# Kernel optimization log

Hardware: AMD Instinct MI355X
Metric: run time of the kernel (lower is better)

The kernel has to match this reference:

```python
import jax, jax.numpy as jnp
import numpy as np

D = 256; NH = 8; NL = 4; NP = 8; DFF = 1024; NQ = 300; BS = 8
DH = D // NH
_SHAPES = np.array([[100, 100], [50, 50], [25, 25], [13, 13]], dtype=np.int64)
S = int(_SHAPES.prod(1).sum())


def setup_inputs():
    key = jax.random.key(0)
    ks = jax.random.split(key, 24)
    rn = lambda k, sh, s=0.02: jax.random.normal(k, sh, jnp.float32) * s
    lsi = np.concatenate([[0], np.cumsum(_SHAPES.prod(1))[:-1]])
    return {
        'tgt': rn(ks[0], (NQ, BS, D), 1.0),
        'tgt_query_mask': rn(ks[1], (NQ, BS, D), 1.0),
        'tgt_reference_bboxs': jax.random.uniform(ks[2], (NQ, BS, 4), jnp.float32, 0.1, 0.5),
        'tgt_reference_masks': jax.random.uniform(ks[3], (NQ, BS, 32, 32), jnp.float32),
        'memory': rn(ks[4], (S, BS, D), 1.0),
        'in_proj_w': rn(ks[5], (3 * D, D)), 'in_proj_b': jnp.zeros((3 * D,), jnp.float32),
        'out_sa_w': rn(ks[6], (D, D)), 'out_sa_b': jnp.zeros((D,), jnp.float32),
        'norm2_g': jnp.ones((D,), jnp.float32), 'norm2_b': jnp.zeros((D,), jnp.float32),
        'value_w': rn(ks[7], (D, D)), 'value_b': jnp.zeros((D,), jnp.float32),
        'off_w': rn(ks[8], (NH * NL * NP * 2, D)), 'off_b': rn(ks[9], (NH * NL * NP * 2,), 0.5),
        'aw_w': rn(ks[10], (NH * NL * NP, D)), 'aw_b': jnp.zeros((NH * NL * NP,), jnp.float32),
        'out_ca_w': rn(ks[11], (D, D)), 'out_ca_b': jnp.zeros((D,), jnp.float32),
        'norm1_g': jnp.ones((D,), jnp.float32), 'norm1_b': jnp.zeros((D,), jnp.float32),
        'lin1_w': rn(ks[12], (DFF, D)), 'lin1_b': jnp.zeros((DFF,), jnp.float32),
        'lin2_w': rn(ks[13], (D, DFF)), 'lin2_b': jnp.zeros((D,), jnp.float32),
        'norm3_g': jnp.ones((D,), jnp.float32), 'norm3_b': jnp.zeros((D,), jnp.float32),
        'memory_key_padding_mask': jnp.zeros((BS, S), bool),
        'memory_spatial_shapes': jnp.asarray(_SHAPES, jnp.int32),
        'memory_level_start_index': jnp.asarray(lsi, jnp.int32),
    }


def _lin(x, w, b):
    return x @ w.T + b


def _ln(x, g, b):
    mu = x.mean(-1, keepdims=True)
    v = ((x - mu) ** 2).mean(-1, keepdims=True)
    return (x - mu) / jnp.sqrt(v + 1e-5) * g + b


def _ms_deform(query, ref, mem, pad_mask, spatial, lstart, vw, vb, ow, ob, aww, awb, outw, outb):
    # query/ref/mem: (bs, nq, D), (bs, nq, 4 cxcywh in [0,1]), (bs, S, D)
    bs, nq, _ = query.shape
    value = _lin(mem, vw, vb)
    value = jnp.where(pad_mask[:, :, None], 0.0, value).reshape(bs, -1, NH, DH)
    off = _lin(query, ow, ob).reshape(bs, nq, NH, NL, NP, 2)
    aw = jax.nn.softmax(_lin(query, aww, awb).reshape(bs, nq, NH, NL * NP), -1)
    aw = aw.reshape(bs, nq, NH, NL, NP)
    ref6 = ref[:, :, None, None, None, :]
    loc = ref6[..., :2] + off / NP * ref6[..., 2:4] * 0.5  # (bs,nq,NH,NL,NP,2)
    Hs = spatial[:, 0].reshape(1, 1, 1, NL, 1)
    Ws = spatial[:, 1].reshape(1, 1, 1, NL, 1)
    ls = lstart.reshape(1, 1, 1, NL, 1)
    Hf = Hs.astype(jnp.float32); Wf = Ws.astype(jnp.float32)
    # grid_sample align_corners=False pixel coords
    x = loc[..., 0] * Wf - 0.5
    y = loc[..., 1] * Hf - 0.5
    x0 = jnp.floor(x); y0 = jnp.floor(y)
    vT = value.transpose(2, 0, 1, 3)  # (NH,bs,S,DH)
    acc = jnp.zeros((bs, nq, NH, NL, NP, DH), jnp.float32)
    for dx in (0.0, 1.0):
        for dy in (0.0, 1.0):
            xi = x0 + dx; yi = y0 + dy
            w = (1.0 - jnp.abs(x - xi)) * (1.0 - jnp.abs(y - yi))
            valid = ((xi >= 0) & (xi < Wf) & (yi >= 0) & (yi < Hf)).astype(jnp.float32)
            xc = jnp.clip(xi, 0.0, Wf - 1.0).astype(jnp.int32)
            yc = jnp.clip(yi, 0.0, Hf - 1.0).astype(jnp.int32)
            idx = ls + yc * Ws + xc  # flat index into S, (bs,nq,NH,NL,NP)
            iT = idx.transpose(2, 0, 1, 3, 4).reshape(NH, bs, -1)
            g = jax.vmap(lambda v, i: jnp.take_along_axis(v, i[:, :, None], axis=1))(vT, iT)
            g = g.reshape(NH, bs, nq, NL, NP, DH).transpose(1, 2, 0, 3, 4, 5)
            acc = acc + (w * valid)[..., None] * g
    out = (acc * aw[..., None]).sum(axis=(3, 4)).reshape(bs, nq, D)
    return _lin(out, outw, outb)


def reference(tgt, tgt_query_mask, tgt_reference_bboxs, tgt_reference_masks, memory,
              in_proj_w, in_proj_b, out_sa_w, out_sa_b, norm2_g, norm2_b,
              value_w, value_b, off_w, off_b, aw_w, aw_b, out_ca_w, out_ca_b,
              norm1_g, norm1_b, lin1_w, lin1_b, lin2_w, lin2_b, norm3_g, norm3_b,
              memory_key_padding_mask, memory_spatial_shapes, memory_level_start_index):
    nq, bs, _ = tgt.shape
    # --- self attention (nn.MultiheadAttention, seq-first, eval mode) ---
    q = tgt + tgt_query_mask
    qh = _lin(q, in_proj_w[:D], in_proj_b[:D]).reshape(nq, bs, NH, DH)
    kh = _lin(q, in_proj_w[D:2 * D], in_proj_b[D:2 * D]).reshape(nq, bs, NH, DH)
    vh = _lin(tgt, in_proj_w[2 * D:], in_proj_b[2 * D:]).reshape(nq, bs, NH, DH)
    logits = jnp.einsum('qbhd,kbhd->bhqk', qh, kh) / np.sqrt(DH).astype(np.float32)
    attn = jax.nn.softmax(logits, -1)
    sa = jnp.einsum('bhqk,kbhd->qbhd', attn, vh).reshape(nq, bs, D)
    sa = _lin(sa, out_sa_w, out_sa_b)
    tgt = _ln(tgt + sa, norm2_g, norm2_b)
    # --- multi-scale deformable cross attention ---
    ca = _ms_deform((tgt + tgt_query_mask).transpose(1, 0, 2),
                    tgt_reference_bboxs.transpose(1, 0, 2),
                    memory.transpose(1, 0, 2),
                    memory_key_padding_mask, memory_spatial_shapes, memory_level_start_index,
                    value_w, value_b, off_w, off_b, aw_w, aw_b, out_ca_w, out_ca_b)
    tgt = _ln(tgt + ca.transpose(1, 0, 2), norm1_g, norm1_b)
    # --- FFN ---
    t2 = _lin(jax.nn.relu(_lin(tgt, lin1_w, lin1_b)), lin2_w, lin2_b)
    return _ln(tgt + t2, norm3_g, norm3_b)
```

## Files before the change

kernel.cpp:

```cpp
#include <hip/hip_runtime.h>
#include <hip/hip_bf16.h>
#include <math.h>

#define NQ 300
#define BSZ 8
#define DIM 256
#define NHEAD 8
#define ROWS 2400

typedef __attribute__((ext_vector_type(8))) short bf16x8;
typedef __attribute__((ext_vector_type(4))) float f32x4;

__device__ inline short f2bf(float f) {
  __hip_bfloat16 h = __float2bfloat16(f);
  return *reinterpret_cast<short*>(&h);
}
__device__ inline float bf2f(unsigned short u) {
  union { unsigned u; float f; } c;
  c.u = ((unsigned)u) << 16;
  return c.f;
}
__device__ inline bf16x8 cvt8(float4 v0, float4 v1) {
  bf16x8 o;
  o[0] = f2bf(v0.x); o[1] = f2bf(v0.y); o[2] = f2bf(v0.z); o[3] = f2bf(v0.w);
  o[4] = f2bf(v1.x); o[5] = f2bf(v1.y); o[6] = f2bf(v1.z); o[7] = f2bf(v1.w);
  return o;
}

struct WEntry { const float* src; unsigned short* dst; int K; int gstart; };
struct WPack { WEntry e[8]; int total; };
__global__ __launch_bounds__(256) void wconv_kernel(WPack P) {
  int g = blockIdx.x * 256 + threadIdx.x;
  if (g >= P.total) return;
  int i = 0;
  while (i < 7 && g >= P.e[i + 1].gstart) ++i;
  int gl = g - P.e[i].gstart;
  const float* s = P.e[i].src + (size_t)gl * 8;
  float4 v0 = *(const float4*)s, v1 = *(const float4*)(s + 4);
  ((bf16x8*)P.e[i].dst)[gl] = cvt8(v0, v1);
}

__global__ void bias_cat(const float* __restrict__ a, const float* __restrict__ b,
                         float* __restrict__ o) {
  int t = blockIdx.x * 256 + threadIdx.x;
  if (t < 512) o[t] = a[t];
  else if (t < 768) o[t] = b[t - 512];
}

template <bool VMASK>
__global__ __launch_bounds__(512) void vgemm(const float* __restrict__ A,
                                             const unsigned short* __restrict__ Wb,
                                             const float* __restrict__ bias,
                                             __hip_bfloat16* __restrict__ C, int M,
                                             const unsigned char* __restrict__ vmask,
                                             int Srows) {
  __shared__ char As[2][16384];
  const int tid = threadIdx.x, lane = tid & 63, wid = tid >> 6;
  const int wr = wid >> 2, wc = wid & 3;
  const int nb = blockIdx.x;
  const int m0 = blockIdx.y * 128;
  const int l15 = lane & 15, lk = lane >> 4;

  f32x4 acc[4][2];
#pragma unroll
  for (int i = 0; i < 4; ++i)
#pragma unroll
    for (int j = 0; j < 2; ++j) acc[i][j] = {0.f, 0.f, 0.f, 0.f};

  const float* asrc[2];
  int awby[2];
#pragma unroll
  for (int j = 0; j < 2; ++j) {
    int gb = j * 512 + tid;
    int row = gb >> 3, g8 = gb & 7;
    int rg = m0 + row;
    if (rg > M - 1) rg = M - 1;
    asrc[j] = A + (size_t)rg * 256 + g8 * 8;
    awby[j] = row * 128 + ((g8 * 16) ^ ((row & 7) << 4));
  }
  const char* bsrc[2];
#pragma unroll
  for (int j = 0; j < 2; ++j) {
    int rr = nb * 128 + wc * 32 + j * 16 + l15;
    bsrc[j] = (const char*)Wb + (size_t)rr * 512 + lk * 16;
  }

  float4 ar[4];
#define V_AISSUE(c)                                 \
  {                                                 \
    _Pragma("unroll") for (int j = 0; j < 2; ++j) { \
      const float* p = asrc[j] + (c) * 64;          \
      ar[2 * j] = *(const float4*)p;                \
      ar[2 * j + 1] = *(const float4*)(p + 4);      \
    }                                               \
  }
#define V_AWRITE(buf)                                                  \
  {                                                                    \
    _Pragma("unroll") for (int j = 0; j < 2; ++j)                      \
        *(bf16x8*)((buf) + awby[j]) = cvt8(ar[2 * j], ar[2 * j + 1]);  \
  }
#define V_COMPUTE(Ab, c)                                                         \
  {                                                                              \
    _Pragma("unroll") for (int kk = 0; kk < 2; ++kk) {                           \
      bf16x8 af[4], bfr[2];                                                      \
      _Pragma("unroll") for (int j = 0; j < 2; ++j)                              \
          bfr[j] = *(const bf16x8*)(bsrc[j] + (c) * 128 + kk * 64);              \
      _Pragma("unroll") for (int i = 0; i < 4; ++i) {                            \
        int rr = wr * 64 + i * 16 + l15;                                         \
        af[i] = *(bf16x8*)((Ab) + rr * 128 + (((kk * 4 + lk) * 16) ^ ((rr & 7) << 4))); \
      }                                                                          \
      _Pragma("unroll") for (int i = 0; i < 4; ++i)                              \
          _Pragma("unroll") for (int j = 0; j < 2; ++j)                          \
              acc[i][j] = __builtin_amdgcn_mfma_f32_16x16x32_bf16(af[i], bfr[j], \
                                                                  acc[i][j], 0, 0, 0); \
    }                                                                            \
  }

  V_AISSUE(0);
  V_AWRITE(As[0]);
  __syncthreads();
#pragma unroll
  for (int c = 0; c < 4; ++c) {
    const int cur = c & 1;
    if (c < 3) V_AISSUE(c + 1);
    V_COMPUTE(As[cur], c);
    if (c < 3) {
      V_AWRITE(As[cur ^ 1]);
      __syncthreads();
    }
  }

#pragma unroll
  for (int i = 0; i < 4; ++i) {
#pragma unroll
    for (int r = 0; r < 4; ++r) {
      int row = m0 + wr * 64 + i * 16 + lk * 4 + r;
      if (row >= M) continue;
      float mfac = 1.f;
      if (VMASK) mfac = vmask[(size_t)(row & 7) * Srows + (row >> 3)] ? 0.f : 1.f;
#pragma unroll
      for (int j = 0; j < 2; ++j) {
        int col = nb * 128 + wc * 32 + j * 16 + l15;
        float v = acc[i][j][r] + bias[col];
        if (VMASK) v *= mfac;
        C[(size_t)row * 256 + col] = __float2bfloat16(v);
      }
    }
  }
}

template <int BM, bool RELU, bool ADDM, bool QKV>
__global__ __launch_bounds__(256) void sgemm(const float* __restrict__ A,
                                             const float* __restrict__ Am,
                                             const unsigned short* __restrict__ Wb,
                                             const float* __restrict__ bias,
                                             float* __restrict__ C0, float* __restrict__ C1,
                                             int M, int Ns, int K) {
  constexpr int WMT = BM / 2, AM = WMT / 16, NA = BM / 32;
  __shared__ char As[2][BM * 128];
  const int tid = threadIdx.x, lane = tid & 63, wid = tid >> 6;
  const int wr = wid >> 1, wc = wid & 1;
  const int nb = blockIdx.x, m0 = blockIdx.y * BM;
  const int l15 = lane & 15, lk = lane >> 4;
  const bool useM = QKV ? (nb < 8) : ADDM;

  f32x4 acc[AM][2];
#pragma unroll
  for (int i = 0; i < AM; ++i)
#pragma unroll
    for (int j = 0; j < 2; ++j) acc[i][j] = {0.f, 0.f, 0.f, 0.f};

  const int nch = K >> 6;
  const float* asrc[NA];
  const float* amsrc[NA];
  int awby[NA];
  bool avalid[NA];
#pragma unroll
  for (int j = 0; j < NA; ++j) {
    int gb = j * 256 + tid;
    int row = gb >> 3, g8 = gb & 7;
    int rg = m0 + row;
    avalid[j] = rg < M;
    if (rg > M - 1) rg = M - 1;
    asrc[j] = A + (size_t)rg * K + g8 * 8;
    amsrc[j] = (useM ? Am : A) + (size_t)rg * K + g8 * 8;
    awby[j] = row * 128 + ((g8 * 16) ^ ((row & 7) << 4));
  }
  const char* bsrc[2];
#pragma unroll
  for (int j = 0; j < 2; ++j) {
    int rr = nb * 64 + wc * 32 + j * 16 + l15;
    bsrc[j] = (const char*)Wb + (size_t)rr * (K * 2) + lk * 16;
  }

  float4 ar[2 * NA], am2[2 * NA];
#define S_AISSUE(c)                                          \
  {                                                          \
    _Pragma("unroll") for (int j = 0; j < NA; ++j) {         \
      const float* p = asrc[j] + (c) * 64;                   \
      ar[2 * j] = *(const float4*)p;                         \
      ar[2 * j + 1] = *(const float4*)(p + 4);               \
      if (useM) {                                            \
        const float* q = amsrc[j] + (c) * 64;                \
        am2[2 * j] = *(const float4*)q;                      \
        am2[2 * j + 1] = *(const float4*)(q + 4);            \
      }                                                      \
    }                                                        \
  }
#define S_AWRITE(buf)                                                       \
  {                                                                         \
    _Pragma("unroll") for (int j = 0; j < NA; ++j) {                        \
      float4 v0 = ar[2 * j], v1 = ar[2 * j + 1];                            \
      if (useM) {                                                           \
        float4 w0 = am2[2 * j], w1 = am2[2 * j + 1];                        \
        v0.x += w0.x; v0.y += w0.y; v0.z += w0.z; v0.w += w0.w;             \
        v1.x += w1.x; v1.y += w1.y; v1.z += w1.z; v1.w += w1.w;             \
      }                                                                     \
      if (!avalid[j]) { v0 = make_float4(0.f,0.f,0.f,0.f); v1 = v0; }       \
      *(bf16x8*)((buf) + awby[j]) = cvt8(v0, v1);                           \
    }                                                                       \
  }
#define S_COMPUTE(Ab, c)                                                         \
  {                                                                              \
    _Pragma("unroll") for (int kk = 0; kk < 2; ++kk) {                           \
      bf16x8 af[AM], bfr[2];                                                     \
      _Pragma("unroll") for (int j = 0; j < 2; ++j)                              \
          bfr[j] = *(const bf16x8*)(bsrc[j] + (c) * 128 + kk * 64);              \
      _Pragma("unroll") for (int i = 0; i < AM; ++i) {                           \
        int rr = wr * WMT + i * 16 + l15;                                        \
        af[i] = *(bf16x8*)((Ab) + rr * 128 + (((kk * 4 + lk) * 16) ^ ((rr & 7) << 4))); \
      }                                                                          \
      _Pragma("unroll") for (int i = 0; i < AM; ++i)                             \
          _Pragma("unroll") for (int j = 0; j < 2; ++j)                          \
              acc[i][j] = __builtin_amdgcn_mfma_f32_16x16x32_bf16(af[i], bfr[j], \
                                                                  acc[i][j], 0, 0, 0); \
    }                                                                            \
  }

  S_AISSUE(0);
  S_AWRITE(As[0]);
  __syncthreads();
  for (int c = 0; c < nch; ++c) {
    const int cur = c & 1;
    if (c < nch - 1) S_AISSUE(c + 1);
    S_COMPUTE(As[cur], c);
    if (c < nch - 1) {
      S_AWRITE(As[cur ^ 1]);
      __syncthreads();
    }
  }

  float* outp;
  int ostride, ocol0;
  if (QKV) {
    if (nb < 8) { outp = C0; ostride = 512; ocol0 = nb * 64; }
    else        { outp = C1; ostride = 256; ocol0 = (nb - 8) * 64; }
  } else {
    outp = C0; ostride = Ns; ocol0 = nb * 64;
  }
#pragma unroll
  for (int i = 0; i < AM; ++i) {
#pragma unroll
    for (int r = 0; r < 4; ++r) {
      int row = m0 + wr * WMT + i * 16 + lk * 4 + r;
      if (row >= M) continue;
#pragma unroll
      for (int j = 0; j < 2; ++j) {
        int cl = wc * 32 + j * 16 + l15;
        float v = acc[i][j][r] + bias[nb * 64 + cl];
        if (RELU) v = fmaxf(v, 0.f);
        outp[(size_t)row * ostride + ocol0 + cl] = v;
      }
    }
  }
}

__global__ __launch_bounds__(256) void attn_kernel(const float* __restrict__ cqk,
                                                   const float* __restrict__ cv,
                                                   float* __restrict__ out) {
  __shared__ float Ks[NQ][32];
  __shared__ float Vs[NQ][32];
  const int b = blockIdx.x, h = blockIdx.y, qt = blockIdx.z;
  const int tid = threadIdx.x;
  for (int i = tid; i < NQ * 8; i += 256) {
    int qi = i >> 3, c4 = (i & 7) * 4;
    *(float4*)&Ks[qi][c4] = *(const float4*)&cqk[((size_t)(qi * 8 + b)) * 512 + 256 + h * 32 + c4];
    *(float4*)&Vs[qi][c4] = *(const float4*)&cv[((size_t)(qi * 8 + b)) * 256 + h * 32 + c4];
  }
  __syncthreads();
  const int row = qt * 64 + (tid >> 2);
  const int qr = tid & 3;
  if (row >= NQ) return;
  float qv[8];
  const float* qptr = &cqk[((size_t)(row * 8 + b)) * 512 + h * 32 + qr * 8];
  *(float4*)&qv[0] = *(const float4*)&qptr[0];
  *(float4*)&qv[4] = *(const float4*)&qptr[4];
  const float scale = 0.17677669529663687f;
  float m = -3.0e38f, l = 0.f;
  float acc[8] = {0.f, 0.f, 0.f, 0.f, 0.f, 0.f, 0.f, 0.f};
  for (int k = 0; k < NQ; ++k) {
    const float* kr = &Ks[k][qr * 8];
    float p = 0.f;
#pragma unroll
    for (int j = 0; j < 8; ++j) p = fmaf(qv[j], kr[j], p);
    p += __shfl_xor(p, 1, 4);
    p += __shfl_xor(p, 2, 4);
    float s = p * scale;
    float mn = fmaxf(m, s);
    float corr = __expf(m - mn);
    float e = __expf(s - mn);
    l = l * corr + e;
    const float* vr = &Vs[k][qr * 8];
#pragma unroll
    for (int j = 0; j < 8; ++j) acc[j] = fmaf(acc[j], corr, e * vr[j]);
    m = mn;
  }
  float inv = 1.f / l;
  float* op = &out[((size_t)(row * 8 + b)) * 256 + h * 32 + qr * 8];
#pragma unroll
  for (int j = 0; j < 8; ++j) op[j] = acc[j] * inv;
}

__global__ __launch_bounds__(256) void resid_ln_kernel(const float* __restrict__ X,
                                                       const float* __restrict__ R,
                                                       const float* __restrict__ g,
                                                       const float* __restrict__ be,
                                                       float* __restrict__ out) {
  const int r = blockIdx.x, c = threadIdx.x;
  const size_t i = (size_t)r * 256 + c;
  float x = X[i] + R[i];
  float s = x;
#pragma unroll
  for (int o = 32; o; o >>= 1) s += __shfl_xor(s, o, 64);
  __shared__ float sm[4], sv[4];
  const int w = c >> 6;
  if ((c & 63) == 0) sm[w] = s;
  __syncthreads();
  float mu = (sm[0] + sm[1] + sm[2] + sm[3]) * (1.f / 256.f);
  float d = x - mu;
  float v = d * d;
#pragma unroll
  for (int o = 32; o; o >>= 1) v += __shfl_xor(v, o, 64);
  if ((c & 63) == 0) sv[w] = v;
  __syncthreads();
  float var = (sv[0] + sv[1] + sv[2] + sv[3]) * (1.f / 256.f);
  out[i] = d * (1.f / sqrtf(var + 1e-5f)) * g[c] + be[c];
}

__global__ __launch_bounds__(256) void deform_kernel(const unsigned short* __restrict__ value,
                                                     const float* __restrict__ offaw,
                                                     const float* __restrict__ bbox,
                                                     const int* __restrict__ spatial,
                                                     const int* __restrict__ lstart,
                                                     float* __restrict__ out, int S) {
  __shared__ int sH[4], sW[4], sL[4];
  __shared__ float sbb[4];
  const int r = blockIdx.x;
  const int b = r & 7;
  const int tid = threadIdx.x;
  if (tid < 4) {
    sH[tid] = spatial[tid * 2];
    sW[tid] = spatial[tid * 2 + 1];
    sL[tid] = lstart[tid];
    sbb[tid] = bbox[(size_t)r * 4 + tid];
  }
  __syncthreads();
  const float cx = sbb[0], cy = sbb[1], bw = sbb[2], bh = sbb[3];
  float ox = offaw[(size_t)r * 768 + (size_t)tid * 2];
  float oy = offaw[(size_t)r * 768 + (size_t)tid * 2 + 1];
  float a = offaw[(size_t)r * 768 + 512 + tid];
  float mx = a;
#pragma unroll
  for (int o = 16; o; o >>= 1) mx = fmaxf(mx, __shfl_xor(mx, o, 32));
  float e = __expf(a - mx);
  float ssum = e;
#pragma unroll
  for (int o = 16; o; o >>= 1) ssum += __shfl_xor(ssum, o, 32);
  float myaw = e / ssum;

  float acc = 0.f;
  const size_t vb = (size_t)b * 256 + (size_t)tid;
  for (int lp = 0; lp < 32; ++lp) {
    const int l = lp >> 3;
    float bx = __shfl(ox, lp, 32);
    float by = __shfl(oy, lp, 32);
    float alp = __shfl(myaw, lp, 32);
    const float Wf = (float)sW[l], Hf = (float)sH[l];
    const int ls = sL[l], Wi = sW[l];
    float lx = cx + bx * 0.0625f * bw;
    float ly = cy + by * 0.0625f * bh;
    float x = lx * Wf - 0.5f;
    float y = ly * Hf - 0.5f;
    float x0 = floorf(x), y0 = floorf(y);
    float fx = x - x0, fy = y - y0;
    float tap = 0.f;
#pragma unroll
    for (int t = 0; t < 4; ++t) {
      float xi = x0 + (float)(t & 1);
      float yi = y0 + (float)(t >> 1);
      if (xi >= 0.f && yi >= 0.f && xi < Wf && yi < Hf) {
        float wx = (t & 1) ? fx : (1.f - fx);
        float wy = (t >> 1) ? fy : (1.f - fy);
        int idx = ls + (int)yi * Wi + (int)xi;
        tap = fmaf(wx * wy, bf2f(value[(size_t)idx * 2048 + vb]), tap);
      }
    }
    acc = fmaf(alp, tap, acc);
  }
  out[(size_t)r * 256 + tid] = acc;
}

extern "C" void kernel_launch(void* const* d_in, const int* in_sizes, int n_in, void* d_out,
                              int out_size, void* d_ws, size_t ws_size, hipStream_t stream) {
  (void)n_in; (void)out_size; (void)ws_size;
  const float* tgt = (const float*)d_in[0];
  const float* qmask = (const float*)d_in[1];
  const float* bbox = (const float*)d_in[2];
  const float* memory = (const float*)d_in[4];
  const float* ipw = (const float*)d_in[5];
  const float* ipb = (const float*)d_in[6];
  const float* osw = (const float*)d_in[7];
  const float* osb = (const float*)d_in[8];
  const float* n2g = (const float*)d_in[9];
  const float* n2b = (const float*)d_in[10];
  const float* vw = (const float*)d_in[11];
  const float* vbi = (const float*)d_in[12];
  const float* ow = (const float*)d_in[13];
  const float* ob = (const float*)d_in[14];
  const float* aww = (const float*)d_in[15];
  const float* awb = (const float*)d_in[16];
  const float* ocw = (const float*)d_in[17];
  const float* ocb = (const float*)d_in[18];
  const float* n1g = (const float*)d_in[19];
  const float* n1b = (const float*)d_in[20];
  const float* l1w = (const float*)d_in[21];
  const float* l1b = (const float*)d_in[22];
  const float* l2w = (const float*)d_in[23];
  const float* l2b = (const float*)d_in[24];
  const float* n3g = (const float*)d_in[25];
  const float* n3b = (const float*)d_in[26];
  const unsigned char* kpmask = (const unsigned char*)d_in[27];
  const int* spatial = (const int*)d_in[28];
  const int* lstart = (const int*)d_in[29];
  float* out = (float*)d_out;

  const int S = in_sizes[4] / (BSZ * DIM);
  const int Mv = S * BSZ;

  float* ws = (float*)d_ws;
  size_t o = 0;
  unsigned short* value = (unsigned short*)(ws + o); o += (size_t)Mv * DIM / 2;
  float* cqk = ws + o; o += (size_t)ROWS * 512;
  float* cv = ws + o; o += (size_t)ROWS * DIM;
  float* sraw = ws + o; o += (size_t)ROWS * DIM;
  float* proj = ws + o; o += (size_t)ROWS * DIM;
  float* tgt2 = ws + o; o += (size_t)ROWS * DIM;
  float* tgt3 = ws + o; o += (size_t)ROWS * DIM;
  float* ffn1 = ws + o; o += (size_t)ROWS * 1024;
  float* offaw = ws + o; o += (size_t)ROWS * 768;
  float* obaw = ws + o; o += 768;
  unsigned short* wz = (unsigned short*)(ws + o);
  unsigned short* ipw_z = wz;
  unsigned short* osw_z = ipw_z + 768 * 256;
  unsigned short* vw_z  = osw_z + 256 * 256;
  unsigned short* ow_z  = vw_z + 256 * 256;
  unsigned short* aww_z = ow_z + 512 * 256;
  unsigned short* ocw_z = aww_z + 256 * 256;
  unsigned short* l1w_z = ocw_z + 256 * 256;
  unsigned short* l2w_z = l1w_z + 1024 * 256;

  WPack P;
  int gs = 0;
  auto ent = [&](int idx, const float* s, unsigned short* d, int N_, int K_) {
    P.e[idx] = {s, d, K_, gs};
    gs += N_ * K_ / 8;
  };
  ent(0, ipw, ipw_z, 768, 256);
  ent(1, osw, osw_z, 256, 256);
  ent(2, vw, vw_z, 256, 256);
  ent(3, ow, ow_z, 512, 256);
  ent(4, aww, aww_z, 256, 256);
  ent(5, ocw, ocw_z, 256, 256);
  ent(6, l1w, l1w_z, 1024, 256);
  ent(7, l2w, l2w_z, 256, 1024);
  P.total = gs;
  wconv_kernel<<<dim3((gs + 255) / 256), 256, 0, stream>>>(P);
  bias_cat<<<dim3(3), 256, 0, stream>>>(ob, awb, obaw);

  sgemm<64, false, false, true><<<dim3(12, 38), 256, 0, stream>>>(
      tgt, qmask, ipw_z, ipb, cqk, cv, ROWS, 0, 256);
  attn_kernel<<<dim3(BSZ, NHEAD, (NQ + 63) / 64), 256, 0, stream>>>(cqk, cv, sraw);
  sgemm<32, false, false, false><<<dim3(4, 75), 256, 0, stream>>>(
      sraw, nullptr, osw_z, osb, proj, nullptr, ROWS, 256, 256);
  resid_ln_kernel<<<ROWS, 256, 0, stream>>>(proj, tgt, n2g, n2b, tgt2);
  vgemm<true><<<dim3(2, (Mv + 127) / 128), 512, 0, stream>>>(
      memory, vw_z, vbi, (__hip_bfloat16*)value, Mv, kpmask, S);
  sgemm<64, false, true, false><<<dim3(12, 38), 256, 0, stream>>>(
      tgt2, qmask, ow_z, obaw, offaw, nullptr, ROWS, 768, 256);
  deform_kernel<<<ROWS, 256, 0, stream>>>(value, offaw, bbox, spatial, lstart, sraw, S);
  sgemm<32, false, false, false><<<dim3(4, 75), 256, 0, stream>>>(
      sraw, nullptr, ocw_z, ocb, proj, nullptr, ROWS, 256, 256);
  resid_ln_kernel<<<ROWS, 256, 0, stream>>>(proj, tgt2, n1g, n1b, tgt3);
  sgemm<64, true, false, false><<<dim3(16, 38), 256, 0, stream>>>(
      tgt3, nullptr, l1w_z, l1b, ffn1, nullptr, ROWS, 1024, 256);
  sgemm<32, false, false, false><<<dim3(4, 75), 256, 0, stream>>>(
      ffn1, nullptr, l2w_z, l2b, proj, nullptr, ROWS, 256, 1024);
  resid_ln_kernel<<<ROWS, 256, 0, stream>>>(proj, tgt3, n3g, n3b, out);
}
```

Baseline: 455.9 us.

## Deepen GEMM A-prefetch and move query-mask adds out of GEMM loaders

The sgemm kernel now takes K as a template constant (NCH chunks) and keeps up to four A chunks in flight in registers instead of one, and vgemm issues all four A chunks up front. The tgt+query_mask add is taken out of the GEMM loaders: a separate elementwise add produces the summed query for QKV, and the norm2 LayerNorm also writes tgt2+qmask for the offset/attention-weight GEMM. The intent is to hide global-load latency and simplify the loader. In exchange it adds a kernel launch, extra intermediate buffers and traffic, and higher register pressure from the larger prefetch arrays.

```diff
diff --git a/kernel.cpp b/kernel.cpp
--- a/kernel.cpp
+++ b/kernel.cpp
@@ -25,6 +25,16 @@
   o[0] = f2bf(v0.x); o[1] = f2bf(v0.y); o[2] = f2bf(v0.z); o[3] = f2bf(v0.w);
   o[4] = f2bf(v1.x); o[5] = f2bf(v1.y); o[6] = f2bf(v1.z); o[7] = f2bf(v1.w);
   return o;
+}
+
+__global__ __launch_bounds__(256) void add4_kernel(const float4* __restrict__ a,
+                                                   const float4* __restrict__ b,
+                                                   float4* __restrict__ o, int n4) {
+  int i = blockIdx.x * 256 + threadIdx.x;
+  if (i < n4) {
+    float4 x = a[i], y = b[i];
+    o[i] = make_float4(x.x + y.x, x.y + y.y, x.z + y.z, x.w + y.w);
+  }
 }
 
 struct WEntry { const float* src; unsigned short* dst; int K; int gstart; };
@@ -85,19 +95,20 @@
     bsrc[j] = (const char*)Wb + (size_t)rr * 512 + lk * 16;
   }
 
-  float4 ar[4];
-#define V_AISSUE(c)                                 \
-  {                                                 \
-    _Pragma("unroll") for (int j = 0; j < 2; ++j) { \
-      const float* p = asrc[j] + (c) * 64;          \
-      ar[2 * j] = *(const float4*)p;                \
-      ar[2 * j + 1] = *(const float4*)(p + 4);      \
-    }                                               \
-  }
-#define V_AWRITE(buf)                                                  \
-  {                                                                    \
-    _Pragma("unroll") for (int j = 0; j < 2; ++j)                      \
-        *(bf16x8*)((buf) + awby[j]) = cvt8(ar[2 * j], ar[2 * j + 1]);  \
+  float4 ar[4][4];
+#pragma unroll
+  for (int c = 0; c < 4; ++c)
+#pragma unroll
+    for (int j = 0; j < 2; ++j) {
+      const float* sp_ = asrc[j] + c * 64;
+      ar[c][2 * j] = *(const float4*)sp_;
+      ar[c][2 * j + 1] = *(const float4*)(sp_ + 4);
+    }
+
+#define V_AWRITE(buf, c)                                                     \
+  {                                                                          \
+    _Pragma("unroll") for (int j = 0; j < 2; ++j)                            \
+        *(bf16x8*)((buf) + awby[j]) = cvt8(ar[c][2 * j], ar[c][2 * j + 1]);  \
   }
 #define V_COMPUTE(Ab, c)                                                         \
   {                                                                              \
@@ -116,16 +127,13 @@
     }                                                                            \
   }
 
-  V_AISSUE(0);
-  V_AWRITE(As[0]);
+  V_AWRITE(As[0], 0);
   __syncthreads();
 #pragma unroll
   for (int c = 0; c < 4; ++c) {
-    const int cur = c & 1;
-    if (c < 3) V_AISSUE(c + 1);
-    V_COMPUTE(As[cur], c);
+    V_COMPUTE(As[c & 1], c);
     if (c < 3) {
-      V_AWRITE(As[cur ^ 1]);
+      V_AWRITE(As[(c + 1) & 1], c + 1);
       __syncthreads();
     }
   }
@@ -149,20 +157,21 @@
   }
 }
 
-template <int BM, bool RELU, bool ADDM, bool QKV>
+template <int NCH, int BM, bool RELU, bool QKV>
 __global__ __launch_bounds__(256) void sgemm(const float* __restrict__ A,
-                                             const float* __restrict__ Am,
+                                             const float* __restrict__ A2,
                                              const unsigned short* __restrict__ Wb,
                                              const float* __restrict__ bias,
                                              float* __restrict__ C0, float* __restrict__ C1,
-                                             int M, int Ns, int K) {
+                                             int M, int Ns) {
   constexpr int WMT = BM / 2, AM = WMT / 16, NA = BM / 32;
+  constexpr int K = NCH * 64;
+  constexpr int PF = NCH < 4 ? NCH : 4;
   __shared__ char As[2][BM * 128];
   const int tid = threadIdx.x, lane = tid & 63, wid = tid >> 6;
   const int wr = wid >> 1, wc = wid & 1;
   const int nb = blockIdx.x, m0 = blockIdx.y * BM;
   const int l15 = lane & 15, lk = lane >> 4;
-  const bool useM = QKV ? (nb < 8) : ADDM;
 
   f32x4 acc[AM][2];
 #pragma unroll
@@ -170,20 +179,16 @@
 #pragma unroll
     for (int j = 0; j < 2; ++j) acc[i][j] = {0.f, 0.f, 0.f, 0.f};
 
-  const int nch = K >> 6;
+  const float* Abase = QKV ? (nb < 8 ? A : A2) : A;
   const float* asrc[NA];
-  const float* amsrc[NA];
   int awby[NA];
-  bool avalid[NA];
 #pragma unroll
   for (int j = 0; j < NA; ++j) {
     int gb = j * 256 + tid;
     int row = gb >> 3, g8 = gb & 7;
     int rg = m0 + row;
-    avalid[j] = rg < M;
     if (rg > M - 1) rg = M - 1;
-    asrc[j] = A + (size_t)rg * K + g8 * 8;
-    amsrc[j] = (useM ? Am : A) + (size_t)rg * K + g8 * 8;
+    asrc[j] = Abase + (size_t)rg * K + g8 * 8;
     awby[j] = row * 128 + ((g8 * 16) ^ ((row & 7) << 4));
   }
   const char* bsrc[2];
@@ -193,32 +198,19 @@
     bsrc[j] = (const char*)Wb + (size_t)rr * (K * 2) + lk * 16;
   }
 
-  float4 ar[2 * NA], am2[2 * NA];
-#define S_AISSUE(c)                                          \
+  float4 ar[4][2 * NA];
+#define S_AISSUE(c, s)                                       \
   {                                                          \
     _Pragma("unroll") for (int j = 0; j < NA; ++j) {         \
-      const float* p = asrc[j] + (c) * 64;                   \
-      ar[2 * j] = *(const float4*)p;                         \
-      ar[2 * j + 1] = *(const float4*)(p + 4);               \
-      if (useM) {                                            \
-        const float* q = amsrc[j] + (c) * 64;                \
-        am2[2 * j] = *(const float4*)q;                      \
-        am2[2 * j + 1] = *(const float4*)(q + 4);            \
-      }                                                      \
+      const float* sp_ = asrc[j] + (c) * 64;                 \
+      ar[s][2 * j] = *(const float4*)sp_;                    \
+      ar[s][2 * j + 1] = *(const float4*)(sp_ + 4);          \
     }                                                        \
   }
-#define S_AWRITE(buf)                                                       \
-  {                                                                         \
-    _Pragma("unroll") for (int j = 0; j < NA; ++j) {                        \
-      float4 v0 = ar[2 * j], v1 = ar[2 * j + 1];                            \
-      if (useM) {                                                           \
-        float4 w0 = am2[2 * j], w1 = am2[2 * j + 1];                        \
-        v0.x += w0.x; v0.y += w0.y; v0.z += w0.z; v0.w += w0.w;             \
-        v1.x += w1.x; v1.y += w1.y; v1.z += w1.z; v1.w += w1.w;             \
-      }                                                                     \
-      if (!avalid[j]) { v0 = make_float4(0.f,0.f,0.f,0.f); v1 = v0; }       \
-      *(bf16x8*)((buf) + awby[j]) = cvt8(v0, v1);                           \
-    }                                                                       \
+#define S_AWRITE(buf, s)                                                        \
+  {                                                                             \
+    _Pragma("unroll") for (int j = 0; j < NA; ++j)                              \
+        *(bf16x8*)((buf) + awby[j]) = cvt8(ar[s][2 * j], ar[s][2 * j + 1]);     \
   }
 #define S_COMPUTE(Ab, c)                                                         \
   {                                                                              \
@@ -237,15 +229,16 @@
     }                                                                            \
   }
 
-  S_AISSUE(0);
-  S_AWRITE(As[0]);
+#pragma unroll
+  for (int p = 0; p < PF; ++p) S_AISSUE(p, p & 3);
+  S_AWRITE(As[0], 0);
   __syncthreads();
-  for (int c = 0; c < nch; ++c) {
-    const int cur = c & 1;
-    if (c < nch - 1) S_AISSUE(c + 1);
-    S_COMPUTE(As[cur], c);
-    if (c < nch - 1) {
-      S_AWRITE(As[cur ^ 1]);
+#pragma unroll
+  for (int c = 0; c < NCH; ++c) {
+    if (c + 4 < NCH) S_AISSUE(c + 4, c & 3);
+    S_COMPUTE(As[c & 1], c);
+    if (c + 1 < NCH) {
+      S_AWRITE(As[(c + 1) & 1], (c + 1) & 3);
       __syncthreads();
     }
   }
@@ -325,7 +318,9 @@
                                                        const float* __restrict__ R,
                                                        const float* __restrict__ g,
                                                        const float* __restrict__ be,
-                                                       float* __restrict__ out) {
+                                                       const float* __restrict__ addmask,
+                                                       float* __restrict__ out,
+                                                       float* __restrict__ out2) {
   const int r = blockIdx.x, c = threadIdx.x;
   const size_t i = (size_t)r * 256 + c;
   float x = X[i] + R[i];
@@ -344,7 +339,9 @@
   if ((c & 63) == 0) sv[w] = v;
   __syncthreads();
   float var = (sv[0] + sv[1] + sv[2] + sv[3]) * (1.f / 256.f);
-  out[i] = d * (1.f / sqrtf(var + 1e-5f)) * g[c] + be[c];
+  float y = d * (1.f / sqrtf(var + 1e-5f)) * g[c] + be[c];
+  out[i] = y;
+  if (out2) out2[i] = y + addmask[i];
 }
 
 __global__ __launch_bounds__(256) void deform_kernel(const unsigned short* __restrict__ value,
@@ -450,11 +447,13 @@
   float* ws = (float*)d_ws;
   size_t o = 0;
   unsigned short* value = (unsigned short*)(ws + o); o += (size_t)Mv * DIM / 2;
+  float* qsum = ws + o; o += (size_t)ROWS * DIM;
   float* cqk = ws + o; o += (size_t)ROWS * 512;
   float* cv = ws + o; o += (size_t)ROWS * DIM;
   float* sraw = ws + o; o += (size_t)ROWS * DIM;
   float* proj = ws + o; o += (size_t)ROWS * DIM;
   float* tgt2 = ws + o; o += (size_t)ROWS * DIM;
+  float* q2 = ws + o; o += (size_t)ROWS * DIM;
   float* tgt3 = ws + o; o += (size_t)ROWS * DIM;
   float* ffn1 = ws + o; o += (size_t)ROWS * 1024;
   float* offaw = ws + o; o += (size_t)ROWS * 768;
@@ -487,23 +486,25 @@
   wconv_kernel<<<dim3((gs + 255) / 256), 256, 0, stream>>>(P);
   bias_cat<<<dim3(3), 256, 0, stream>>>(ob, awb, obaw);
 
-  sgemm<64, false, false, true><<<dim3(12, 38), 256, 0, stream>>>(
-      tgt, qmask, ipw_z, ipb, cqk, cv, ROWS, 0, 256);
+  add4_kernel<<<dim3((ROWS * DIM / 4 + 255) / 256), 256, 0, stream>>>(
+      (const float4*)tgt, (const float4*)qmask, (float4*)qsum, ROWS * DIM / 4);
+  sgemm<4, 64, false, true><<<dim3(12, 38), 256, 0, stream>>>(
+      qsum, tgt, ipw_z, ipb, cqk, cv, ROWS, 0);
   attn_kernel<<<dim3(BSZ, NHEAD, (NQ + 63) / 64), 256, 0, stream>>>(cqk, cv, sraw);
-  sgemm<32, false, false, false><<<dim3(4, 75), 256, 0, stream>>>(
-      sraw, nullptr, osw_z, osb, proj, nullptr, ROWS, 256, 256);
-  resid_ln_kernel<<<ROWS, 256, 0, stream>>>(proj, tgt, n2g, n2b, tgt2);
+  sgemm<4, 32, false, false><<<dim3(4, 75), 256, 0, stream>>>(
+      sraw, nullptr, osw_z, osb, proj, nullptr, ROWS, 256);
+  resid_ln_kernel<<<ROWS, 256, 0, stream>>>(proj, tgt, n2g, n2b, qmask, tgt2, q2);
   vgemm<true><<<dim3(2, (Mv + 127) / 128), 512, 0, stream>>>(
       memory, vw_z, vbi, (__hip_bfloat16*)value, Mv, kpmask, S);
-  sgemm<64, false, true, false><<<dim3(12, 38), 256, 0, stream>>>(
-      tgt2, qmask, ow_z, obaw, offaw, nullptr, ROWS, 768, 256);
+  sgemm<4, 64, false, false><<<dim3(12, 38), 256, 0, stream>>>(
+      q2, nullptr, ow_z, obaw, offaw, nullptr, ROWS, 768);
   deform_kernel<<<ROWS, 256, 0, stream>>>(value, offaw, bbox, spatial, lstart, sraw, S);
-  sgemm<32, false, false, false><<<dim3(4, 75), 256, 0, stream>>>(
-      sraw, nullptr, ocw_z, ocb, proj, nullptr, ROWS, 256, 256);
-  resid_ln_kernel<<<ROWS, 256, 0, stream>>>(proj, tgt2, n1g, n1b, tgt3);
-  sgemm<64, true, false, false><<<dim3(16, 38), 256, 0, stream>>>(
-      tgt3, nullptr, l1w_z, l1b, ffn1, nullptr, ROWS, 1024, 256);
-  sgemm<32, false, false, false><<<dim3(4, 75), 256, 0, stream>>>(
-      ffn1, nullptr, l2w_z, l2b, proj, nullptr, ROWS, 256, 1024);
-  resid_ln_kernel<<<ROWS, 256, 0, stream>>>(proj, tgt3, n3g, n3b, out);
-}
+  sgemm<4, 32, false, false><<<dim3(4, 75), 256, 0, stream>>>(
+      sraw, nullptr, ocw_z, ocb, proj, nullptr, ROWS, 256);
+  resid_ln_kernel<<<ROWS, 256, 0, stream>>>(proj, tgt2, n1g, n1b, nullptr, tgt3, nullptr);
+  sgemm<4, 64, true, false><<<dim3(16, 38), 256, 0, stream>>>(
+      tgt3, nullptr, l1w_z, l1b, ffn1, nullptr, ROWS, 1024);
+  sgemm<16, 32, false, false><<<dim3(4, 75), 256, 0, stream>>>(
+      ffn1, nullptr, l2w_z, l2b, proj, nullptr, ROWS, 256);
+  resid_ln_kernel<<<ROWS, 256, 0, stream>>>(proj, tgt3, n3g, n3b, nullptr, out, nullptr);
+}
```

After: 451.9 us. No clear change (-0.9%).
